# Kernel optimization log

Measured on AMD Instinct MI355X. Metric: run time of the kernel, lower is better.

The kernel has to match this reference:

```python
import jax, jax.numpy as jnp
import numpy as np

N = 50000      # nodes
E = 1600000    # edges
F_IN = 128     # input_dim
H = 160        # hidden_dim
G = 512        # graphs in batch
C = 2          # num_classes
EPS = 1e-5     # BatchNorm eps


def setup_inputs() -> dict:
    key = jax.random.key(0)
    ks = jax.random.split(key, 12)
    x = jax.random.normal(ks[0], (N, F_IN), jnp.float32)
    edge_index = jax.random.randint(ks[1], (2, E), 0, N, dtype=jnp.int32)
    batch = jnp.sort(jax.random.randint(ks[2], (N,), 0, G, dtype=jnp.int32))

    def lin(k, fi, fo):
        s = 1.0 / np.sqrt(fi)
        kw, kb = jax.random.split(k)
        W = jax.random.uniform(kw, (fi, fo), jnp.float32, -s, s)
        b = jax.random.uniform(kb, (fo,), jnp.float32, -s, s)
        return W, b

    W1, b1 = lin(ks[3], F_IN, H)
    W2, b2 = lin(ks[4], H, H)
    W3, b3 = lin(ks[5], H, H)
    Wc1, bc1 = lin(ks[6], H, H // 2)
    Wc2, bc2 = lin(ks[7], H // 2, C)

    def bn(k):
        k1, k2, k3, k4 = jax.random.split(k, 4)
        gamma = jax.random.uniform(k1, (H,), jnp.float32, 0.5, 1.5)
        beta = jax.random.normal(k2, (H,), jnp.float32) * 0.1
        mean = jax.random.normal(k3, (H,), jnp.float32) * 0.1
        var = jax.random.uniform(k4, (H,), jnp.float32, 0.5, 1.5)
        return gamma, beta, mean, var

    g1, be1, m1, v1 = bn(ks[8])
    g2, be2, m2, v2 = bn(ks[9])
    g3, be3, m3, v3 = bn(ks[10])

    return dict(x=x, edge_index=edge_index, batch=batch,
                W1=W1, b1=b1, W2=W2, b2=b2, W3=W3, b3=b3,
                g1=g1, be1=be1, m1=m1, v1=v1,
                g2=g2, be2=be2, m2=m2, v2=v2,
                g3=g3, be3=be3, m3=m3, v3=v3,
                Wc1=Wc1, bc1=bc1, Wc2=Wc2, bc2=bc2)


def gcn_conv(x, W, b, src, dst):
    """PyG GCNConv: symmetric deg normalization with self-loops; lin -> aggregate -> +bias."""
    n = x.shape[0]
    h = x @ W                                   # [N, H]
    loop = jnp.arange(n, dtype=src.dtype)
    s = jnp.concatenate([src, loop])            # self-loops appended
    d = jnp.concatenate([dst, loop])
    deg = jax.ops.segment_sum(jnp.ones_like(d, jnp.float32), d, num_segments=n)
    inv = jnp.where(deg > 0, jax.lax.rsqrt(deg), 0.0)
    msg = h[s] * (inv[s] * inv[d])[:, None]     # [E+N, H] gather + norm
    return jax.ops.segment_sum(msg, d, num_segments=n) + b


def bn_eval(x, gamma, beta, mean, var):
    return (x - mean) * jax.lax.rsqrt(var + EPS) * gamma + beta


def reference(x, edge_index, batch, W1, b1, W2, b2, W3, b3,
              g1, be1, m1, v1, g2, be2, m2, v2, g3, be3, m3, v3,
              Wc1, bc1, Wc2, bc2):
    src, dst = edge_index[0], edge_index[1]
    # eval mode: dropout is identity, BN uses running stats
    h = jax.nn.relu(bn_eval(gcn_conv(x, W1, b1, src, dst), g1, be1, m1, v1))
    h = jax.nn.relu(bn_eval(gcn_conv(h, W2, b2, src, dst), g2, be2, m2, v2))
    h = jax.nn.relu(bn_eval(gcn_conv(h, W3, b3, src, dst), g3, be3, m3, v3))
    # global mean pool over graph ids
    sums = jax.ops.segment_sum(h, batch, num_segments=G)
    cnt = jax.ops.segment_sum(jnp.ones((h.shape[0],), jnp.float32), batch, num_segments=G)
    pooled = sums / jnp.clip(cnt, 1.0)[:, None]
    # MLP head
    z = jax.nn.relu(pooled @ Wc1 + bc1)
    return z @ Wc2 + bc2
```

## Files before the change

kernel.cpp:

```cpp
#include <hip/hip_runtime.h>

#define N_NODES   50000
#define N_EDGES   1600000
#define FDIM_IN   128
#define HDIM      160
#define N_GRAPHS  512
#define BN_EPS    1e-5f
#define NBKT_MAX  128

typedef short  frag8 __attribute__((ext_vector_type(8)));
typedef float  facc4 __attribute__((ext_vector_type(4)));


__device__ __forceinline__ unsigned short f2bf(float f) {
    unsigned int u = __float_as_uint(f);
    return (unsigned short)((u + 0x7FFFu + ((u >> 16) & 1u)) >> 16);
}

__device__ __forceinline__ unsigned int pack2(float lo, float hi) {
    return (unsigned int)f2bf(lo) | ((unsigned int)f2bf(hi) << 16);
}

__device__ __forceinline__ void addpk(float* acc, uint4 r) {
    acc[0] += __uint_as_float(r.x << 16);
    acc[1] += __uint_as_float(r.x & 0xFFFF0000u);
    acc[2] += __uint_as_float(r.y << 16);
    acc[3] += __uint_as_float(r.y & 0xFFFF0000u);
    acc[4] += __uint_as_float(r.z << 16);
    acc[5] += __uint_as_float(r.z & 0xFFFF0000u);
    acc[6] += __uint_as_float(r.w << 16);
    acc[7] += __uint_as_float(r.w & 0xFFFF0000u);
}


__global__ __launch_bounds__(256) void coarse_hist_kernel(const int* __restrict__ dst,
                                                          int* __restrict__ cg, int E) {
    __shared__ int h[NBKT_MAX];
    int tid = threadIdx.x;
    if (tid < NBKT_MAX) h[tid] = 0;
    __syncthreads();
    for (int e = blockIdx.x * 256 + tid; e < E; e += gridDim.x * 256)
        atomicAdd(&h[dst[e] >> 9], 1);
    __syncthreads();
    if (tid < NBKT_MAX && h[tid]) atomicAdd(&cg[tid], h[tid]);
}

__global__ __launch_bounds__(128) void coarse_scan_kernel(const int* __restrict__ cg,
                                                          int* __restrict__ bucket_base,
                                                          int* __restrict__ bucket_cursor) {
    __shared__ int h[NBKT_MAX];
    int t = threadIdx.x;
    h[t] = cg[t];
    __syncthreads();
    if (t == 0) {
        int run = 0;
        for (int i = 0; i < NBKT_MAX; ++i) { int c = h[i]; h[i] = run; run += c; }
    }
    __syncthreads();
    bucket_base[t] = h[t];
    bucket_cursor[t] = h[t];
    if (t == 0) bucket_base[NBKT_MAX] = h[NBKT_MAX - 1] + cg[NBKT_MAX - 1];
}

__global__ __launch_bounds__(256) void part_kernel(const int* __restrict__ src,
                                                   const int* __restrict__ dst,
                                                   int* __restrict__ bucket_cursor,
                                                   unsigned int* __restrict__ pairs, int E) {
    __shared__ int bcnt[NBKT_MAX], bbase[NBKT_MAX], lc[NBKT_MAX];
    int tid = threadIdx.x;
    int per = (E + gridDim.x - 1) / gridDim.x;
    int beg = blockIdx.x * per;
    int end = min(beg + per, E);
    if (tid < NBKT_MAX) { bcnt[tid] = 0; lc[tid] = 0; }
    __syncthreads();
    for (int e = beg + tid; e < end; e += 256)
        atomicAdd(&bcnt[dst[e] >> 9], 1);
    __syncthreads();
    if (tid < NBKT_MAX)
        bbase[tid] = bcnt[tid] ? atomicAdd(&bucket_cursor[tid], bcnt[tid]) : 0;
    __syncthreads();
    for (int e = beg + tid; e < end; e += 256) {
        int d = dst[e];
        int b = d >> 9;
        int pos = bbase[b] + atomicAdd(&lc[b], 1);
        pairs[pos] = ((unsigned int)src[e] << 9) | (unsigned int)(d & 511);
    }
}

__global__ __launch_bounds__(1024) void bucket_csr_kernel(const unsigned int* __restrict__ pairs,
                                                          const int* __restrict__ bucket_base,
                                                          int* __restrict__ row_off,
                                                          float* __restrict__ inv,
                                                          int* __restrict__ ssrc, int n) {
    __shared__ int h[512];
    __shared__ int ws[8];
    int tid = threadIdx.x;
    int b = blockIdx.x;
    int node0 = b << 9;
    int beg = bucket_base[b], end = bucket_base[b + 1];
    if (tid < 512) h[tid] = 0;
    __syncthreads();
    for (int j = beg + tid; j < end; j += 1024)
        atomicAdd(&h[pairs[j] & 511], 1);
    __syncthreads();
    int cntv = (tid < 512) ? h[tid] : 0;
    __syncthreads();
    int lane = tid & 63, wid = tid >> 6;
    int incl = cntv;
    #pragma unroll
    for (int off = 1; off < 64; off <<= 1) {
        int u = __shfl_up(incl, off);
        if (lane >= off) incl += u;
    }
    if (tid < 512 && lane == 63) ws[wid] = incl;
    __syncthreads();
    if (tid == 0) {
        int r = 0;
        #pragma unroll
        for (int i = 0; i < 8; ++i) { int t = ws[i]; ws[i] = r; r += t; }
    }
    __syncthreads();
    int excl = (tid < 512) ? (ws[wid] + incl - cntv) : 0;
    if (tid < 512) {
        int node = node0 + tid;
        if (node < n) {
            row_off[node] = beg + excl;
            inv[node] = rsqrtf((float)(cntv + 1));
        }
        h[tid] = excl;
    }
    if (tid == 0 && (node0 + 512) >= n) row_off[n] = end;
    __syncthreads();
    for (int j = beg + tid; j < end; j += 1024) {
        unsigned int p = pairs[j];
        int pos = beg + atomicAdd(&h[p & 511], 1);
        ssrc[pos] = (int)(p >> 9);
    }
}


struct PrepArgs {
    const float *b, *g, *be, *m, *v;
    float *sc, *sh;
};

__global__ void prep3_kernel(PrepArgs a0, PrepArgs a1, PrepArgs a2) {
    PrepArgs a = (blockIdx.x == 0) ? a0 : (blockIdx.x == 1) ? a1 : a2;
    int t = threadIdx.x;
    if (t < HDIM) {
        float s = a.g[t] * rsqrtf(a.v[t] + BN_EPS);
        a.sc[t] = s;
        a.sh[t] = (a.b[t] - a.m[t]) * s + a.be[t];
    }
}


__global__ __launch_bounds__(256) void pack_w3_kernel(const float* __restrict__ W1,
                                                      const float* __restrict__ W2,
                                                      const float* __restrict__ W3,
                                                      unsigned short* __restrict__ o1,
                                                      unsigned short* __restrict__ o2,
                                                      unsigned short* __restrict__ o3) {
    int tid = blockIdx.x * 256 + threadIdx.x;
    const float* W;
    unsigned short* o;
    int i;
    if (tid < 128 * 160)             { W = W1; o = o1; i = tid; }
    else if (tid < 128 * 160 + 160 * 160) { W = W2; o = o2; i = tid - 128 * 160; }
    else if (tid < 128 * 160 + 2 * 160 * 160) { W = W3; o = o3; i = tid - (128 * 160 + 160 * 160); }
    else return;
    int j = i & 7;
    int l = (i >> 3) & 63;
    int u = (i >> 9) % 10;
    int t = i / 5120;
    int k = t * 32 + (l >> 4) * 8 + j;
    int nn = u * 16 + (l & 15);
    o[i] = f2bf(W[k * 160 + nn]);
}


__global__ __launch_bounds__(256) void scale_bf16_kernel(const float* __restrict__ x,
                                                         const float* __restrict__ inv,
                                                         unsigned short* __restrict__ out,
                                                         int n) {
    int i = blockIdx.x * 256 + threadIdx.x;
    if (i < n * 32) {
        int node = i >> 5;
        float w = inv[node];
        float4 v = ((const float4*)x)[i];
        ushort4 o;
        o.x = f2bf(v.x * w); o.y = f2bf(v.y * w);
        o.z = f2bf(v.z * w); o.w = f2bf(v.w * w);
        ((ushort4*)out)[i] = o;
    }
}


template <int C>
__global__ __launch_bounds__(256) void agg_grp_kernel(const unsigned short* __restrict__ in_s,
                                                      const float* __restrict__ inv,
                                                      const int* __restrict__ row_off,
                                                      const int* __restrict__ ssrc,
                                                      unsigned short* __restrict__ out, int n) {
    constexpr int LPR = C / 8;
    constexpr int G   = 64 / LPR;
    constexpr int RB  = C * 2;
    int wave = threadIdx.x >> 6;
    int lane = threadIdx.x & 63;
    int node = blockIdx.x * 4 + wave;
    if (node >= n) return;
    int g  = lane / LPR;
    int cl = lane - g * LPR;
    bool act = g < G;
    int beg = row_off[node], end = row_off[node + 1];
    const char* base = (const char*)in_s;
    int lb = cl * 16;

    float acc[8];
    #pragma unroll
    for (int i = 0; i < 8; ++i) acc[i] = 0.f;

    if (g == 0) {
        uint4 r = *(const uint4*)(base + (size_t)node * RB + lb);
        addpk(acc, r);
    }

    int e = act ? beg + g : end;

    for (; e + 7 * G < end; e += 8 * G) {
        int s0 = ssrc[e],         s1 = ssrc[e + G];
        int s2 = ssrc[e + 2 * G], s3 = ssrc[e + 3 * G];
        int s4 = ssrc[e + 4 * G], s5 = ssrc[e + 5 * G];
        int s6 = ssrc[e + 6 * G], s7 = ssrc[e + 7 * G];
        uint4 r0 = *(const uint4*)(base + (size_t)s0 * RB + lb);
        uint4 r1 = *(const uint4*)(base + (size_t)s1 * RB + lb);
        uint4 r2 = *(const uint4*)(base + (size_t)s2 * RB + lb);
        uint4 r3 = *(const uint4*)(base + (size_t)s3 * RB + lb);
        uint4 r4 = *(const uint4*)(base + (size_t)s4 * RB + lb);
        uint4 r5 = *(const uint4*)(base + (size_t)s5 * RB + lb);
        uint4 r6 = *(const uint4*)(base + (size_t)s6 * RB + lb);
        uint4 r7 = *(const uint4*)(base + (size_t)s7 * RB + lb);
        addpk(acc, r0); addpk(acc, r1); addpk(acc, r2); addpk(acc, r3);
        addpk(acc, r4); addpk(acc, r5); addpk(acc, r6); addpk(acc, r7);
    }
    if (e + 3 * G < end) {
        int s0 = ssrc[e],         s1 = ssrc[e + G];
        int s2 = ssrc[e + 2 * G], s3 = ssrc[e + 3 * G];
        uint4 r0 = *(const uint4*)(base + (size_t)s0 * RB + lb);
        uint4 r1 = *(const uint4*)(base + (size_t)s1 * RB + lb);
        uint4 r2 = *(const uint4*)(base + (size_t)s2 * RB + lb);
        uint4 r3 = *(const uint4*)(base + (size_t)s3 * RB + lb);
        addpk(acc, r0); addpk(acc, r1); addpk(acc, r2); addpk(acc, r3);
        e += 4 * G;
    }
    if (e + G < end) {
        int s0 = ssrc[e], s1 = ssrc[e + G];
        uint4 r0 = *(const uint4*)(base + (size_t)s0 * RB + lb);
        uint4 r1 = *(const uint4*)(base + (size_t)s1 * RB + lb);
        addpk(acc, r0); addpk(acc, r1);
        e += 2 * G;
    }
    if (e < end) {
        uint4 r = *(const uint4*)(base + (size_t)ssrc[e] * RB + lb);
        addpk(acc, r);
    }

    if (G == 4) {
        #pragma unroll
        for (int i = 0; i < 8; ++i) acc[i] += __shfl(acc[i], lane + 32);
        #pragma unroll
        for (int i = 0; i < 8; ++i) acc[i] += __shfl(acc[i], lane + 16);
    } else {
        #pragma unroll
        for (int i = 0; i < 8; ++i) {
            float a = __shfl(acc[i], lane + 20);
            float b = __shfl(acc[i], lane + 40);
            acc[i] += a + b;
        }
    }

    if (lane < LPR) {
        float wi = inv[node];
        uint4 o;
        o.x = pack2(acc[0] * wi, acc[1] * wi);
        o.y = pack2(acc[2] * wi, acc[3] * wi);
        o.z = pack2(acc[4] * wi, acc[5] * wi);
        o.w = pack2(acc[6] * wi, acc[7] * wi);
        *(uint4*)((char*)out + (size_t)node * RB + lb) = o;
    }
}


template <int K, int OUTMODE>
__global__ __launch_bounds__(256) void mfma_gemm_kernel(const unsigned short* __restrict__ A,
                                                        const unsigned short* __restrict__ Bp,
                                                        const float* __restrict__ sc,
                                                        const float* __restrict__ sh,
                                                        const float* __restrict__ inv,
                                                        float* __restrict__ CoutF,
                                                        unsigned short* __restrict__ CoutB,
                                                        int n) {
    constexpr int KT = K / 32;
    int tid = threadIdx.x;
    int wave = tid >> 6, lane = tid & 63;
    int row0 = blockIdx.x * 64 + wave * 16;
    int m = lane & 15, q = lane >> 4;

    int arow = row0 + m;
    int arowc = (arow < n) ? arow : (n - 1);
    const frag8* Abase = (const frag8*)(A + (size_t)arowc * K);
    const frag8* Bbase = (const frag8*)Bp;

    facc4 acc[10];
    #pragma unroll
    for (int u = 0; u < 10; ++u) acc[u] = (facc4){0.f, 0.f, 0.f, 0.f};

    #pragma unroll
    for (int t = 0; t < KT; ++t) {
        frag8 af = Abase[t * 4 + q];
        #pragma unroll
        for (int u = 0; u < 10; ++u) {
            frag8 bf = Bbase[(t * 10 + u) * 64 + lane];
            acc[u] = __builtin_amdgcn_mfma_f32_16x16x32_bf16(af, bf, acc[u], 0, 0, 0);
        }
    }

    #pragma unroll
    for (int u = 0; u < 10; ++u) {
        int c = u * 16 + m;
        float scv = sc[c], shv = sh[c];
        #pragma unroll
        for (int r = 0; r < 4; ++r) {
            int rr = row0 + q * 4 + r;
            if (rr < n) {
                float v = fmaxf(acc[u][r] * scv + shv, 0.f);
                if (OUTMODE == 1) {
                    CoutB[(size_t)rr * 160 + c] = f2bf(v * inv[rr]);
                } else {
                    CoutF[(size_t)rr * 160 + c] = v;
                }
            }
        }
    }
}


__global__ __launch_bounds__(256) void pool_head_kernel(const float* __restrict__ h,
                                                        const int* __restrict__ batch,
                                                        const float* __restrict__ Wc1,
                                                        const float* __restrict__ bc1,
                                                        const float* __restrict__ Wc2,
                                                        const float* __restrict__ bc2,
                                                        float* __restrict__ out, int n) {
    __shared__ float pooled[160];
    __shared__ float z[80];
    __shared__ int range[2];
    int g = blockIdx.x;
    int t = threadIdx.x;
    if (t < 2) {
        int target = g + t;
        int lo = 0, hi = n;
        while (lo < hi) {
            int mid = (lo + hi) >> 1;
            if (batch[mid] < target) lo = mid + 1; else hi = mid;
        }
        range[t] = lo;
    }
    __syncthreads();
    int lo = range[0], hi = range[1];
    if (t < 160) {
        float s = 0.f;
        for (int r = lo; r < hi; ++r) s += h[(size_t)r * 160 + t];
        pooled[t] = s / fmaxf((float)(hi - lo), 1.f);
    }
    __syncthreads();
    if (t < 80) {
        float s = bc1[t];
        for (int k = 0; k < 160; ++k) s += pooled[k] * Wc1[k * 80 + t];
        z[t] = fmaxf(s, 0.f);
    }
    __syncthreads();
    if (t < 2) {
        float s = bc2[t];
        for (int k = 0; k < 80; ++k) s += z[k] * Wc2[k * 2 + t];
        out[g * 2 + t] = s;
    }
}


static inline size_t align256(size_t x) { return (x + 255) & ~(size_t)255; }

extern "C" void kernel_launch(void* const* d_in, const int* in_sizes, int n_in,
                              void* d_out, int out_size, void* d_ws, size_t ws_size,
                              hipStream_t stream) {
    const float* x   = (const float*)d_in[0];
    const int* ei    = (const int*)d_in[1];
    const int* batch = (const int*)d_in[2];
    const float* W1  = (const float*)d_in[3];
    const float* b1  = (const float*)d_in[4];
    const float* W2  = (const float*)d_in[5];
    const float* b2  = (const float*)d_in[6];
    const float* W3  = (const float*)d_in[7];
    const float* b3  = (const float*)d_in[8];
    const float* g1  = (const float*)d_in[9];
    const float* be1 = (const float*)d_in[10];
    const float* m1  = (const float*)d_in[11];
    const float* v1  = (const float*)d_in[12];
    const float* g2  = (const float*)d_in[13];
    const float* be2 = (const float*)d_in[14];
    const float* m2  = (const float*)d_in[15];
    const float* v2  = (const float*)d_in[16];
    const float* g3  = (const float*)d_in[17];
    const float* be3 = (const float*)d_in[18];
    const float* m3  = (const float*)d_in[19];
    const float* v3  = (const float*)d_in[20];
    const float* Wc1 = (const float*)d_in[21];
    const float* bc1 = (const float*)d_in[22];
    const float* Wc2 = (const float*)d_in[23];
    const float* bc2 = (const float*)d_in[24];
    float* out = (float*)d_out;

    const int N = in_sizes[2];
    const int E = in_sizes[1] / 2;
    const int* src = ei;
    const int* dst = ei + E;

    char* w = (char*)d_ws;
    int*   row_off = (int*)w;             w += align256((size_t)(N + 1) * 4);
    float* inv     = (float*)w;           w += align256((size_t)N * 4);
    int*   ssrc    = (int*)w;             w += align256((size_t)E * 4);
    unsigned int* pairs = (unsigned int*)w; w += align256((size_t)E * 4);
    int*   cg      = (int*)w;             w += align256((size_t)NBKT_MAX * 4);
    int*   bucket_base   = (int*)w;       w += align256((size_t)(NBKT_MAX + 1) * 4);
    int*   bucket_cursor = (int*)w;       w += align256((size_t)NBKT_MAX * 4);
    float* scsh    = (float*)w;           w += align256((size_t)6 * HDIM * 4);
    unsigned short* W1p = (unsigned short*)w;  w += align256((size_t)FDIM_IN * HDIM * 2);
    unsigned short* W2p = (unsigned short*)w;  w += align256((size_t)HDIM * HDIM * 2);
    unsigned short* W3p = (unsigned short*)w;  w += align256((size_t)HDIM * HDIM * 2);
    unsigned short* bufA_bf = (unsigned short*)w;  w += align256((size_t)N * HDIM * 2);
    char* regionR = w;
    unsigned short* xs_bf = (unsigned short*)regionR;
    unsigned short* hs_bf = (unsigned short*)(regionR + align256((size_t)N * FDIM_IN * 2));
    float* bufB = (float*)regionR;
    float* sc1 = scsh, *sh1 = scsh + 160, *sc2 = scsh + 320, *sh2 = scsh + 480,
         * sc3 = scsh + 640, *sh3 = scsh + 800;

    hipMemsetAsync(cg, 0, (size_t)NBKT_MAX * 4, stream);

    coarse_hist_kernel<<<256, 256, 0, stream>>>(dst, cg, E);
    coarse_scan_kernel<<<1, 128, 0, stream>>>(cg, bucket_base, bucket_cursor);
    part_kernel<<<256, 256, 0, stream>>>(src, dst, bucket_cursor, pairs, E);
    int nbkt = (N + 511) >> 9;
    bucket_csr_kernel<<<nbkt, 1024, 0, stream>>>(pairs, bucket_base, row_off, inv, ssrc, N);

    PrepArgs pa0 = {b1, g1, be1, m1, v1, sc1, sh1};
    PrepArgs pa1 = {b2, g2, be2, m2, v2, sc2, sh2};
    PrepArgs pa2 = {b3, g3, be3, m3, v3, sc3, sh3};
    prep3_kernel<<<3, 256, 0, stream>>>(pa0, pa1, pa2);
    pack_w3_kernel<<<(128 * 160 + 2 * 160 * 160 + 255) / 256, 256, 0, stream>>>(W1, W2, W3, W1p, W2p, W3p);

    int gAgg = (N + 3) / 4;
    int gGemm = (N + 63) / 64;

    scale_bf16_kernel<<<(N * 32 + 255) / 256, 256, 0, stream>>>(x, inv, xs_bf, N);
    agg_grp_kernel<128><<<gAgg, 256, 0, stream>>>(xs_bf, inv, row_off, ssrc, bufA_bf, N);
    mfma_gemm_kernel<128, 1><<<gGemm, 256, 0, stream>>>(bufA_bf, W1p, sc1, sh1, inv, nullptr, hs_bf, N);
    agg_grp_kernel<160><<<gAgg, 256, 0, stream>>>(hs_bf, inv, row_off, ssrc, bufA_bf, N);
    mfma_gemm_kernel<160, 1><<<gGemm, 256, 0, stream>>>(bufA_bf, W2p, sc2, sh2, inv, nullptr, hs_bf, N);
    agg_grp_kernel<160><<<gAgg, 256, 0, stream>>>(hs_bf, inv, row_off, ssrc, bufA_bf, N);
    mfma_gemm_kernel<160, 0><<<gGemm, 256, 0, stream>>>(bufA_bf, W3p, sc3, sh3, inv, bufB, nullptr, N);

    pool_head_kernel<<<N_GRAPHS, 256, 0, stream>>>(bufB, batch, Wc1, bc1, Wc2, bc2, out, N);
}
```

Baseline: 470.0 us.

## Merge setup kernels, fuse input scaling into CSR build, shrink gather unroll

Per-block histograms are now written to a partitioned buffer instead of atomically added, which removes the memset. A single setup kernel then reduces and scans them, and also does the BN constant prep and the weight packing, so several small launches become one. The bf16 scaling of x moves into the bucket CSR kernel, which keeps inverse degrees in shared memory, so the standalone scale kernel is gone. The aggregation gather loop drops from 8-way to 2-way unrolling, which lowers register pressure but leaves fewer loads in flight.

```diff
diff --git a/kernel.cpp b/kernel.cpp
--- a/kernel.cpp
+++ b/kernel.cpp
@@ -7,6 +7,7 @@
 #define N_GRAPHS  512
 #define BN_EPS    1e-5f
 #define NBKT_MAX  128
+#define HIST_BLOCKS 256
 
 typedef short  frag8 __attribute__((ext_vector_type(8)));
 typedef float  facc4 __attribute__((ext_vector_type(4)));
@@ -42,24 +43,70 @@
     for (int e = blockIdx.x * 256 + tid; e < E; e += gridDim.x * 256)
         atomicAdd(&h[dst[e] >> 9], 1);
     __syncthreads();
-    if (tid < NBKT_MAX && h[tid]) atomicAdd(&cg[tid], h[tid]);
-}
-
-__global__ __launch_bounds__(128) void coarse_scan_kernel(const int* __restrict__ cg,
-                                                          int* __restrict__ bucket_base,
-                                                          int* __restrict__ bucket_cursor) {
-    __shared__ int h[NBKT_MAX];
+    if (tid < NBKT_MAX) cg[blockIdx.x * NBKT_MAX + tid] = h[tid];
+}
+
+
+struct PrepArgs {
+    const float *b, *g, *be, *m, *v;
+    float *sc, *sh;
+};
+
+__global__ __launch_bounds__(256) void setup_kernel(const int* __restrict__ cg,
+                                                    int* __restrict__ bucket_base,
+                                                    int* __restrict__ bucket_cursor,
+                                                    PrepArgs a0, PrepArgs a1, PrepArgs a2,
+                                                    const float* __restrict__ W1,
+                                                    const float* __restrict__ W2,
+                                                    const float* __restrict__ W3,
+                                                    unsigned short* __restrict__ o1,
+                                                    unsigned short* __restrict__ o2,
+                                                    unsigned short* __restrict__ o3) {
+    int bid = blockIdx.x;
     int t = threadIdx.x;
-    h[t] = cg[t];
-    __syncthreads();
-    if (t == 0) {
-        int run = 0;
-        for (int i = 0; i < NBKT_MAX; ++i) { int c = h[i]; h[i] = run; run += c; }
-    }
-    __syncthreads();
-    bucket_base[t] = h[t];
-    bucket_cursor[t] = h[t];
-    if (t == 0) bucket_base[NBKT_MAX] = h[NBKT_MAX - 1] + cg[NBKT_MAX - 1];
+    if (bid == 0) {
+        __shared__ int h[NBKT_MAX];
+        __shared__ int total;
+        if (t < NBKT_MAX) {
+            int s = 0;
+            for (int b = 0; b < HIST_BLOCKS; ++b) s += cg[b * NBKT_MAX + t];
+            h[t] = s;
+        }
+        __syncthreads();
+        if (t == 0) {
+            int run = 0;
+            for (int i = 0; i < NBKT_MAX; ++i) { int c = h[i]; h[i] = run; run += c; }
+            total = run;
+        }
+        __syncthreads();
+        if (t < NBKT_MAX) {
+            bucket_base[t] = h[t];
+            bucket_cursor[t] = h[t];
+        }
+        if (t == 0) bucket_base[NBKT_MAX] = total;
+    } else if (bid <= 3) {
+        PrepArgs a = (bid == 1) ? a0 : (bid == 2) ? a1 : a2;
+        if (t < HDIM) {
+            float s = a.g[t] * rsqrtf(a.v[t] + BN_EPS);
+            a.sc[t] = s;
+            a.sh[t] = (a.b[t] - a.m[t]) * s + a.be[t];
+        }
+    } else {
+        int i = (bid - 4) * 256 + t;
+        const float* W;
+        unsigned short* o;
+        if (i < 128 * 160)                 { W = W1; o = o1; }
+        else if (i < 128 * 160 + 160 * 160) { W = W2; o = o2; i -= 128 * 160; }
+        else if (i < 128 * 160 + 2 * 160 * 160) { W = W3; o = o3; i -= 128 * 160 + 160 * 160; }
+        else return;
+        int j = i & 7;
+        int l = (i >> 3) & 63;
+        int u = (i >> 9) % 10;
+        int tt = i / 5120;
+        int k = tt * 32 + (l >> 4) * 8 + j;
+        int nn = u * 16 + (l & 15);
+        o[i] = f2bf(W[k * 160 + nn]);
+    }
 }
 
 __global__ __launch_bounds__(256) void part_kernel(const int* __restrict__ src,
@@ -91,9 +138,13 @@
                                                           const int* __restrict__ bucket_base,
                                                           int* __restrict__ row_off,
                                                           float* __restrict__ inv,
-                                                          int* __restrict__ ssrc, int n) {
+                                                          int* __restrict__ ssrc,
+                                                          const float* __restrict__ x,
+                                                          unsigned short* __restrict__ xs,
+                                                          int n) {
     __shared__ int h[512];
     __shared__ int ws[8];
+    __shared__ float sinv[512];
     int tid = threadIdx.x;
     int b = blockIdx.x;
     int node0 = b << 9;
@@ -122,11 +173,13 @@
     __syncthreads();
     int excl = (tid < 512) ? (ws[wid] + incl - cntv) : 0;
     if (tid < 512) {
+        float iv = rsqrtf((float)(cntv + 1));
         int node = node0 + tid;
         if (node < n) {
             row_off[node] = beg + excl;
-            inv[node] = rsqrtf((float)(cntv + 1));
-        }
+            inv[node] = iv;
+        }
+        sinv[tid] = iv;
         h[tid] = excl;
     }
     if (tid == 0 && (node0 + 512) >= n) row_off[n] = end;
@@ -136,62 +189,16 @@
         int pos = beg + atomicAdd(&h[p & 511], 1);
         ssrc[pos] = (int)(p >> 9);
     }
-}
-
-
-struct PrepArgs {
-    const float *b, *g, *be, *m, *v;
-    float *sc, *sh;
-};
-
-__global__ void prep3_kernel(PrepArgs a0, PrepArgs a1, PrepArgs a2) {
-    PrepArgs a = (blockIdx.x == 0) ? a0 : (blockIdx.x == 1) ? a1 : a2;
-    int t = threadIdx.x;
-    if (t < HDIM) {
-        float s = a.g[t] * rsqrtf(a.v[t] + BN_EPS);
-        a.sc[t] = s;
-        a.sh[t] = (a.b[t] - a.m[t]) * s + a.be[t];
-    }
-}
-
-
-__global__ __launch_bounds__(256) void pack_w3_kernel(const float* __restrict__ W1,
-                                                      const float* __restrict__ W2,
-                                                      const float* __restrict__ W3,
-                                                      unsigned short* __restrict__ o1,
-                                                      unsigned short* __restrict__ o2,
-                                                      unsigned short* __restrict__ o3) {
-    int tid = blockIdx.x * 256 + threadIdx.x;
-    const float* W;
-    unsigned short* o;
-    int i;
-    if (tid < 128 * 160)             { W = W1; o = o1; i = tid; }
-    else if (tid < 128 * 160 + 160 * 160) { W = W2; o = o2; i = tid - 128 * 160; }
-    else if (tid < 128 * 160 + 2 * 160 * 160) { W = W3; o = o3; i = tid - (128 * 160 + 160 * 160); }
-    else return;
-    int j = i & 7;
-    int l = (i >> 3) & 63;
-    int u = (i >> 9) % 10;
-    int t = i / 5120;
-    int k = t * 32 + (l >> 4) * 8 + j;
-    int nn = u * 16 + (l & 15);
-    o[i] = f2bf(W[k * 160 + nn]);
-}
-
-
-__global__ __launch_bounds__(256) void scale_bf16_kernel(const float* __restrict__ x,
-                                                         const float* __restrict__ inv,
-                                                         unsigned short* __restrict__ out,
-                                                         int n) {
-    int i = blockIdx.x * 256 + threadIdx.x;
-    if (i < n * 32) {
-        int node = i >> 5;
-        float w = inv[node];
-        float4 v = ((const float4*)x)[i];
-        ushort4 o;
-        o.x = f2bf(v.x * w); o.y = f2bf(v.y * w);
-        o.z = f2bf(v.z * w); o.w = f2bf(v.w * w);
-        ((ushort4*)out)[i] = o;
+    for (int idx = tid; idx < 512 * 32; idx += 1024) {
+        int nd = node0 + (idx >> 5);
+        if (nd < n) {
+            float w = sinv[idx >> 5];
+            float4 v = ((const float4*)x)[(size_t)nd * 32 + (idx & 31)];
+            ushort4 o;
+            o.x = f2bf(v.x * w); o.y = f2bf(v.y * w);
+            o.z = f2bf(v.z * w); o.w = f2bf(v.w * w);
+            ((ushort4*)xs)[(size_t)nd * 32 + (idx & 31)] = o;
+        }
     }
 }
 
@@ -226,39 +233,12 @@
     }
 
     int e = act ? beg + g : end;
-
-    for (; e + 7 * G < end; e += 8 * G) {
-        int s0 = ssrc[e],         s1 = ssrc[e + G];
-        int s2 = ssrc[e + 2 * G], s3 = ssrc[e + 3 * G];
-        int s4 = ssrc[e + 4 * G], s5 = ssrc[e + 5 * G];
-        int s6 = ssrc[e + 6 * G], s7 = ssrc[e + 7 * G];
-        uint4 r0 = *(const uint4*)(base + (size_t)s0 * RB + lb);
-        uint4 r1 = *(const uint4*)(base + (size_t)s1 * RB + lb);
-        uint4 r2 = *(const uint4*)(base + (size_t)s2 * RB + lb);
-        uint4 r3 = *(const uint4*)(base + (size_t)s3 * RB + lb);
-        uint4 r4 = *(const uint4*)(base + (size_t)s4 * RB + lb);
-        uint4 r5 = *(const uint4*)(base + (size_t)s5 * RB + lb);
-        uint4 r6 = *(const uint4*)(base + (size_t)s6 * RB + lb);
-        uint4 r7 = *(const uint4*)(base + (size_t)s7 * RB + lb);
-        addpk(acc, r0); addpk(acc, r1); addpk(acc, r2); addpk(acc, r3);
-        addpk(acc, r4); addpk(acc, r5); addpk(acc, r6); addpk(acc, r7);
-    }
-    if (e + 3 * G < end) {
-        int s0 = ssrc[e],         s1 = ssrc[e + G];
-        int s2 = ssrc[e + 2 * G], s3 = ssrc[e + 3 * G];
-        uint4 r0 = *(const uint4*)(base + (size_t)s0 * RB + lb);
-        uint4 r1 = *(const uint4*)(base + (size_t)s1 * RB + lb);
-        uint4 r2 = *(const uint4*)(base + (size_t)s2 * RB + lb);
-        uint4 r3 = *(const uint4*)(base + (size_t)s3 * RB + lb);
-        addpk(acc, r0); addpk(acc, r1); addpk(acc, r2); addpk(acc, r3);
-        e += 4 * G;
-    }
-    if (e + G < end) {
+    for (; e + G < end; e += 2 * G) {
         int s0 = ssrc[e], s1 = ssrc[e + G];
         uint4 r0 = *(const uint4*)(base + (size_t)s0 * RB + lb);
         uint4 r1 = *(const uint4*)(base + (size_t)s1 * RB + lb);
-        addpk(acc, r0); addpk(acc, r1);
-        e += 2 * G;
+        addpk(acc, r0);
+        addpk(acc, r1);
     }
     if (e < end) {
         uint4 r = *(const uint4*)(base + (size_t)ssrc[e] * RB + lb);
@@ -430,7 +410,7 @@
     float* inv     = (float*)w;           w += align256((size_t)N * 4);
     int*   ssrc    = (int*)w;             w += align256((size_t)E * 4);
     unsigned int* pairs = (unsigned int*)w; w += align256((size_t)E * 4);
-    int*   cg      = (int*)w;             w += align256((size_t)NBKT_MAX * 4);
+    int*   cg      = (int*)w;             w += align256((size_t)HIST_BLOCKS * NBKT_MAX * 4);
     int*   bucket_base   = (int*)w;       w += align256((size_t)(NBKT_MAX + 1) * 4);
     int*   bucket_cursor = (int*)w;       w += align256((size_t)NBKT_MAX * 4);
     float* scsh    = (float*)w;           w += align256((size_t)6 * HDIM * 4);
@@ -445,24 +425,23 @@
     float* sc1 = scsh, *sh1 = scsh + 160, *sc2 = scsh + 320, *sh2 = scsh + 480,
          * sc3 = scsh + 640, *sh3 = scsh + 800;
 
-    hipMemsetAsync(cg, 0, (size_t)NBKT_MAX * 4, stream);
-
-    coarse_hist_kernel<<<256, 256, 0, stream>>>(dst, cg, E);
-    coarse_scan_kernel<<<1, 128, 0, stream>>>(cg, bucket_base, bucket_cursor);
-    part_kernel<<<256, 256, 0, stream>>>(src, dst, bucket_cursor, pairs, E);
-    int nbkt = (N + 511) >> 9;
-    bucket_csr_kernel<<<nbkt, 1024, 0, stream>>>(pairs, bucket_base, row_off, inv, ssrc, N);
+    coarse_hist_kernel<<<HIST_BLOCKS, 256, 0, stream>>>(dst, cg, E);
 
     PrepArgs pa0 = {b1, g1, be1, m1, v1, sc1, sh1};
     PrepArgs pa1 = {b2, g2, be2, m2, v2, sc2, sh2};
     PrepArgs pa2 = {b3, g3, be3, m3, v3, sc3, sh3};
-    prep3_kernel<<<3, 256, 0, stream>>>(pa0, pa1, pa2);
-    pack_w3_kernel<<<(128 * 160 + 2 * 160 * 160 + 255) / 256, 256, 0, stream>>>(W1, W2, W3, W1p, W2p, W3p);
+    int packTotal = 128 * 160 + 2 * 160 * 160;
+    int setupBlocks = 4 + (packTotal + 255) / 256;
+    setup_kernel<<<setupBlocks, 256, 0, stream>>>(cg, bucket_base, bucket_cursor,
+                                                  pa0, pa1, pa2, W1, W2, W3, W1p, W2p, W3p);
+
+    part_kernel<<<256, 256, 0, stream>>>(src, dst, bucket_cursor, pairs, E);
+    int nbkt = (N + 511) >> 9;
+    bucket_csr_kernel<<<nbkt, 1024, 0, stream>>>(pairs, bucket_base, row_off, inv, ssrc, x, xs_bf, N);
 
     int gAgg = (N + 3) / 4;
     int gGemm = (N + 63) / 64;
 
-    scale_bf16_kernel<<<(N * 32 + 255) / 256, 256, 0, stream>>>(x, inv, xs_bf, N);
     agg_grp_kernel<128><<<gAgg, 256, 0, stream>>>(xs_bf, inv, row_off, ssrc, bufA_bf, N);
     mfma_gemm_kernel<128, 1><<<gGemm, 256, 0, stream>>>(bufA_bf, W1p, sc1, sh1, inv, nullptr, hs_bf, N);
     agg_grp_kernel<160><<<gAgg, 256, 0, stream>>>(hs_bf, inv, row_off, ssrc, bufA_bf, N);
```

Result: no change. 466.4 us (-0.7%).
